# Kernel tuning notes

Hardware: AMD Instinct MI355X
Metric: run time of the kernel (lower is better)

Reference implementation:

```python
import jax, jax.numpy as jnp
import numpy as np
import math

HEAD_DIM = 32
N_Q_HEADS = 32
N_KV_HEADS = 8
ROPE_BASE = 10000.0
NEG_INF = -1e9


def _rope_cos_sin(seq_len, dtype):
    inv_freq = 1.0 / (ROPE_BASE ** (jnp.arange(0, HEAD_DIM, 2, dtype=jnp.float32) / HEAD_DIM))
    pos = jnp.arange(seq_len, dtype=jnp.float32)
    freqs = pos[:, None] * inv_freq[None, :]          # [S, D/2]
    emb = jnp.concatenate([freqs, freqs], axis=-1)     # [S, D]
    return jnp.cos(emb).astype(dtype), jnp.sin(emb).astype(dtype)


def _rotate_half(x):
    x1, x2 = jnp.split(x, 2, axis=-1)
    return jnp.concatenate([-x2, x1], axis=-1)


def _apply_rope(x, cos, sin):
    # x: [B, H, S, D]; cos/sin: [S, D]
    return x * cos[None, None] + _rotate_half(x) * sin[None, None]


def setup_inputs() -> dict:
    key = jax.random.key(0)
    ks = jax.random.split(key, 5)
    B, S, D = 2, 2048, 1024
    sc = 1.0 / math.sqrt(D)
    return {
        "hidden_states": jax.random.normal(ks[0], (B, S, D), jnp.float32),
        "attention_mask": jnp.ones((B, S), jnp.int32),
        "Wq": jax.random.normal(ks[1], (1024, 1024), jnp.float32) * sc,
        "Wk": jax.random.normal(ks[2], (256, 1024), jnp.float32) * sc,
        "Wv": jax.random.normal(ks[3], (256, 1024), jnp.float32) * sc,
        "Wo": jax.random.normal(ks[4], (1024, 1024), jnp.float32) * sc,
    }


def reference(hidden_states, attention_mask, Wq, Wk, Wv, Wo):
    B, S, D = hidden_states.shape
    group = N_Q_HEADS // N_KV_HEADS

    q = (hidden_states @ Wq.T).reshape(B, S, N_Q_HEADS, HEAD_DIM).transpose(0, 2, 1, 3)
    k = (hidden_states @ Wk.T).reshape(B, S, N_KV_HEADS, HEAD_DIM).transpose(0, 2, 1, 3)
    v = (hidden_states @ Wv.T).reshape(B, S, N_KV_HEADS, HEAD_DIM).transpose(0, 2, 1, 3)

    cos, sin = _rope_cos_sin(S, q.dtype)
    q = _apply_rope(q, cos, sin)
    k = _apply_rope(k, cos, sin)

    k = jnp.repeat(k, group, axis=1)  # [B, 32, S, D]
    v = jnp.repeat(v, group, axis=1)

    scores = jnp.einsum("bhqd,bhkd->bhqk", q, k) / math.sqrt(HEAD_DIM)

    causal = jnp.tril(jnp.ones((S, S), bool))
    allowed = causal[None, None] & (attention_mask[:, None, None, :] != 0)
    scores = jnp.where(allowed, scores, NEG_INF)

    attn = jax.nn.softmax(scores, axis=-1)
    out = jnp.einsum("bhqk,bhkd->bhqd", attn, v)  # [B, 32, S, 32]
    out = out.transpose(0, 2, 1, 3).reshape(B, S, D)
    return out @ Wo.T
```

## Files before the change

kernel.cpp:

```cpp
#include <hip/hip_runtime.h>

typedef __bf16 bf16x8 __attribute__((ext_vector_type(8)));
typedef __bf16 bf16x4 __attribute__((ext_vector_type(4)));
typedef short short4v __attribute__((ext_vector_type(4)));
typedef float f32x4 __attribute__((ext_vector_type(4)));

__device__ __forceinline__ f32x4 mfma16(bf16x8 a, bf16x8 b, f32x4 c) {
  return __builtin_amdgcn_mfma_f32_16x16x32_bf16(a, b, c, 0, 0, 0);
}

__device__ __forceinline__ f32x4 mfma16k16(bf16x4 a, bf16x4 b, f32x4 c) {
#if __has_builtin(__builtin_amdgcn_mfma_f32_16x16x16bf16_1k)
  short4v as = __builtin_bit_cast(short4v, a);
  short4v bs = __builtin_bit_cast(short4v, b);
  return __builtin_amdgcn_mfma_f32_16x16x16bf16_1k(as, bs, c, 0, 0, 0);
#else
  f32x4 d;
  asm volatile("v_mfma_f32_16x16x16_bf16 %0, %1, %2, %3"
               : "=v"(d)
               : "v"(a), "v"(b), "v"(c));
  return d;
#endif
}

__device__ __forceinline__ float fast_exp2(float x) {
  return __builtin_amdgcn_exp2f(x);
}

typedef const __attribute__((address_space(1))) void gvoid_t;
typedef __attribute__((address_space(3))) void svoid_t;
__device__ __forceinline__ void lds16(const __bf16* g, __bf16* l) {
  __builtin_amdgcn_global_load_lds((gvoid_t*)g, (svoid_t*)l, 16, 0, 0);
}

__global__ __launch_bounds__(256) void prep(const float* __restrict__ hidden,
                                            const float* __restrict__ Wq,
                                            const float* __restrict__ Wk,
                                            const float* __restrict__ Wv,
                                            const float* __restrict__ Wo,
                                            __bf16* __restrict__ hb,
                                            __bf16* __restrict__ Wqkvb,
                                            __bf16* __restrict__ Wob) {
  int q = blockIdx.x * 256 + threadIdx.x;
  const float* src;
  __bf16* dst;
  if (q < 1048576) {
    src = hidden; dst = hb;
  } else if ((q -= 1048576) < 262144) {
    src = Wq; dst = Wqkvb;
  } else if ((q -= 262144) < 65536) {
    src = Wk; dst = Wqkvb + 1048576;
  } else if ((q -= 65536) < 65536) {
    src = Wv; dst = Wqkvb + 1310720;
  } else {
    q -= 65536;
    src = Wo; dst = Wob;
  }
  float4 v = *(const float4*)(src + (size_t)q * 4);
  bf16x4 o = { (__bf16)v.x, (__bf16)v.y, (__bf16)v.z, (__bf16)v.w };
  *(bf16x4*)(dst + (size_t)q * 4) = o;
}

template <bool BF16_OUT>
__global__ __launch_bounds__(256) void gemm_nt(const __bf16* __restrict__ A,
                                               const __bf16* __restrict__ B,
                                               void* __restrict__ Cv, int N) {
  __shared__ __bf16 As[2][128][32];
  __shared__ __bf16 Bs[2][64][32];
  const int m0 = blockIdx.x * 128, n0 = blockIdx.y * 64;
  const int tid = threadIdx.x;
  const int wave = tid >> 6, lane = tid & 63, quad = lane >> 4, l16 = lane & 15;
  const int wr = wave >> 1, wc = wave & 1;
  const int srA = 32 * wave, srB = 16 * wave;
  const __bf16* Ag = A + (size_t)(m0 + srA + (lane >> 2)) * 1024 + (lane & 3) * 8;
  const __bf16* Bg = B + (size_t)(n0 + srB + (lane >> 2)) * 1024 + (lane & 3) * 8;
  f32x4 acc[4][2] = {};

  auto stage = [&](int buf, int k0) {
    lds16(Ag + k0, &As[buf][srA][0]);
    lds16(Ag + 16 * 1024 + k0, &As[buf][srA + 16][0]);
    lds16(Bg + k0, &Bs[buf][srB][0]);
  };
  stage(0, 0);
  __syncthreads();
  int buf = 0;
  for (int k0 = 0; k0 < 1024; k0 += 32) {
    if (k0 + 32 < 1024) stage(buf ^ 1, k0 + 32);
    bf16x8 af[4], bfr[2];
#pragma unroll
    for (int i = 0; i < 4; i++)
      af[i] = *(bf16x8*)&As[buf][64 * wr + 16 * i + l16][quad * 8];
#pragma unroll
    for (int j = 0; j < 2; j++)
      bfr[j] = *(bf16x8*)&Bs[buf][32 * wc + 16 * j + l16][quad * 8];
#pragma unroll
    for (int i = 0; i < 4; i++)
#pragma unroll
      for (int j = 0; j < 2; j++) acc[i][j] = mfma16(af[i], bfr[j], acc[i][j]);
    __syncthreads();
    buf ^= 1;
  }
#pragma unroll
  for (int i = 0; i < 4; i++)
#pragma unroll
    for (int j = 0; j < 2; j++)
#pragma unroll
      for (int r = 0; r < 4; r++) {
        int row = m0 + 64 * wr + 16 * i + quad * 4 + r;
        int col = n0 + 32 * wc + 16 * j + l16;
        if constexpr (BF16_OUT)
          ((__bf16*)Cv)[(size_t)row * N + col] = (__bf16)acc[i][j][r];
        else
          ((float*)Cv)[(size_t)row * N + col] = acc[i][j][r];
      }
}

__global__ __launch_bounds__(256) void ropevt(__bf16* __restrict__ QKV,
                                              __bf16* __restrict__ VT,
                                              const int* __restrict__ amask,
                                              float* __restrict__ maskb) {
  int idx = blockIdx.x * 256 + threadIdx.x;
  if (idx < 2621440) {
    __bf16* base;
    int m, i;
    if (idx < 2097152) {
      m = idx >> 9;
      int h = (idx >> 4) & 31;
      i = idx & 15;
      base = QKV + (size_t)m * 1536 + h * 32;
    } else {
      int j = idx - 2097152;
      m = j >> 7;
      int h = (j >> 4) & 7;
      i = j & 15;
      base = QKV + (size_t)m * 1536 + 1024 + h * 32;
    }
    int s = m & 2047;
    float inv = __expf(-(float)i * 0.5756462732485114f);
    float ang = (float)s * inv;
    float sn, cs;
    __sincosf(ang, &sn, &cs);
    float x0 = (float)base[i];
    float x1 = (float)base[i + 16];
    base[i] = (__bf16)(x0 * cs - x1 * sn);
    base[i + 16] = (__bf16)(x1 * cs + x0 * sn);
  } else {
    int j = idx - 2621440;
    if (j < 4096) maskb[j] = amask[j] ? -16.0f : -1.5e9f;
    int s4 = j & 511;
    int d = (j >> 9) & 31;
    int hb_ = j >> 14;
    int s = s4 * 4;
    int b_ = hb_ >> 3, hkv_ = hb_ & 7;
    const __bf16* src = QKV + (size_t)(b_ * 2048 + s) * 1536 + 1280 + hkv_ * 32 + d;
    bf16x4 ov = { src[0], src[1536], src[3072], src[4608] };
    *(bf16x4*)&VT[((size_t)hb_ * 32 + d) * 2048 + s] = ov;
  }
}

__global__ __launch_bounds__(256, 2) void attn(const __bf16* __restrict__ QKV,
                                               const __bf16* __restrict__ VT,
                                               const float* __restrict__ maskb,
                                               __bf16* __restrict__ Ob) {
  __shared__ __bf16 Ks[2][64][40];
  __shared__ __bf16 Vs[2][32][72];
  const int tid = threadIdx.x;
  const int wave = tid >> 6, lane = tid & 63;
  const int quad = lane >> 4, l16 = lane & 15;
  const int b = blockIdx.z, h = blockIdx.y, hkv = h >> 2;
  const int xp = blockIdx.x;
  const float SC2 = 0.25503472f;

  const int sk_key = tid >> 2, sk_ch = (tid & 3) * 8;
  const int sv_d = tid >> 3, sv_seg = (tid & 7) * 8;
  const __bf16* ksrc = QKV + (size_t)(b * 2048 + sk_key) * 1536 + 1024 + hkv * 32 + sk_ch;
  const __bf16* vsrc = VT + ((size_t)(b * 8 + hkv) * 32 + sv_d) * 2048 + sv_seg;
  const float* mrow = maskb + b * 2048;

  for (int sp = 0; sp < 2; sp++) {
    const int strip = sp ? 15 - xp : xp;
    const int qw = strip * 128 + wave * 32;
    const int q_row0 = qw + l16, q_row1 = qw + 16 + l16;
    const __bf16* qbase = QKV + (size_t)(b * 2048 + qw + l16) * 1536 + h * 32 + quad * 8;
    bf16x8 qf0 = *(const bf16x8*)qbase;
    bf16x8 qf1 = *(const bf16x8*)(qbase + 16 * 1536);

    {
      uint4 kr = *(const uint4*)ksrc;
      uint4 vr = *(const uint4*)vsrc;
      *(uint4*)&Ks[0][sk_key][sk_ch] = kr;
      *(uint4*)&Vs[0][sv_d][sv_seg] = vr;
    }
    __syncthreads();

    f32x4 o00 = {}, o01 = {}, o10 = {}, o11 = {};
    float rs0 = 0.f, rs1 = 0.f;
    int buf = 0;
    const int ntiles = 2 * strip + 2;

    for (int t = 0; t < ntiles; t++) {
      const int kv0 = t << 6;
      const bool more = (t + 1 < ntiles);
      uint4 kr, vr;
      if (more) {
        kr = *(const uint4*)(ksrc + (size_t)(t + 1) * 64 * 1536);
        vr = *(const uint4*)(vsrc + (size_t)(t + 1) * 64);
      }
      if (kv0 <= qw + 31) {
        bf16x8 kf[4];
#pragma unroll
        for (int kt = 0; kt < 4; kt++)
          kf[kt] = *(bf16x8*)&Ks[buf][16 * kt + l16][quad * 8];
        f32x4 s0[4], s1[4];
#pragma unroll
        for (int kt = 0; kt < 4; kt++) {
          f32x4 z = {};
          s0[kt] = mfma16(kf[kt], qf0, z);
          s1[kt] = mfma16(kf[kt], qf1, z);
        }
        bf16x4 pb0[4], pb1[4];
        if (kv0 + 63 <= qw) {
#pragma unroll
          for (int kt = 0; kt < 4; kt++) {
            const int kb = kv0 + 16 * kt + 4 * quad;
            float4 mb = *(const float4*)(mrow + kb);
#pragma unroll
            for (int r = 0; r < 4; r++) {
              float e0 = fast_exp2(fmaf(s0[kt][r], SC2, (&mb.x)[r]));
              float e1 = fast_exp2(fmaf(s1[kt][r], SC2, (&mb.x)[r]));
              rs0 += e0;
              rs1 += e1;
              pb0[kt][r] = (__bf16)e0;
              pb1[kt][r] = (__bf16)e1;
            }
          }
        } else {
#pragma unroll
          for (int kt = 0; kt < 4; kt++) {
            const int kb = kv0 + 16 * kt + 4 * quad;
            float4 mb = *(const float4*)(mrow + kb);
#pragma unroll
            for (int r = 0; r < 4; r++) {
              const int key = kb + r;
              float e0 = fast_exp2(fmaf(s0[kt][r], SC2, (&mb.x)[r]));
              float e1 = fast_exp2(fmaf(s1[kt][r], SC2, (&mb.x)[r]));
              e0 = (key <= q_row0) ? e0 : 0.f;
              e1 = (key <= q_row1) ? e1 : 0.f;
              rs0 += e0;
              rs1 += e1;
              pb0[kt][r] = (__bf16)e0;
              pb1[kt][r] = (__bf16)e1;
            }
          }
        }
#pragma unroll
        for (int kt = 0; kt < 4; kt++) {
          bf16x4 v0 = *(bf16x4*)&Vs[buf][l16][16 * kt + 4 * quad];
          bf16x4 v1 = *(bf16x4*)&Vs[buf][16 + l16][16 * kt + 4 * quad];
          o00 = mfma16k16(v0, pb0[kt], o00);
          o01 = mfma16k16(v1, pb0[kt], o01);
          o10 = mfma16k16(v0, pb1[kt], o10);
          o11 = mfma16k16(v1, pb1[kt], o11);
        }
      }
      if (more) {
        *(uint4*)&Ks[buf ^ 1][sk_key][sk_ch] = kr;
        *(uint4*)&Vs[buf ^ 1][sv_d][sv_seg] = vr;
      }
      __syncthreads();
      buf ^= 1;
    }
    rs0 += __shfl_xor(rs0, 16);
    rs0 += __shfl_xor(rs0, 32);
    rs1 += __shfl_xor(rs1, 16);
    rs1 += __shfl_xor(rs1, 32);
    float inv0 = 1.0f / rs0, inv1 = 1.0f / rs1;
    size_t row0 = (size_t)(b * 2048 + q_row0);
    size_t row1 = (size_t)(b * 2048 + q_row1);
    bf16x4 w00 = { (__bf16)(o00[0] * inv0), (__bf16)(o00[1] * inv0),
                   (__bf16)(o00[2] * inv0), (__bf16)(o00[3] * inv0) };
    bf16x4 w01 = { (__bf16)(o01[0] * inv0), (__bf16)(o01[1] * inv0),
                   (__bf16)(o01[2] * inv0), (__bf16)(o01[3] * inv0) };
    bf16x4 w10 = { (__bf16)(o10[0] * inv1), (__bf16)(o10[1] * inv1),
                   (__bf16)(o10[2] * inv1), (__bf16)(o10[3] * inv1) };
    bf16x4 w11 = { (__bf16)(o11[0] * inv1), (__bf16)(o11[1] * inv1),
                   (__bf16)(o11[2] * inv1), (__bf16)(o11[3] * inv1) };
    *(bf16x4*)&Ob[row0 * 1024 + h * 32 + quad * 4] = w00;
    *(bf16x4*)&Ob[row0 * 1024 + h * 32 + 16 + quad * 4] = w01;
    *(bf16x4*)&Ob[row1 * 1024 + h * 32 + quad * 4] = w10;
    *(bf16x4*)&Ob[row1 * 1024 + h * 32 + 16 + quad * 4] = w11;
  }
}

extern "C" void kernel_launch(void* const* d_in, const int* in_sizes, int n_in,
                              void* d_out, int out_size, void* d_ws, size_t ws_size,
                              hipStream_t stream) {
  const float* hidden = (const float*)d_in[0];
  const int* amask = (const int*)d_in[1];
  const float* Wq = (const float*)d_in[2];
  const float* Wk = (const float*)d_in[3];
  const float* Wv = (const float*)d_in[4];
  const float* Wo = (const float*)d_in[5];
  float* out = (float*)d_out;

  char* p = (char*)d_ws;
  auto carve = [&](size_t elems) {
    __bf16* r = (__bf16*)p;
    p += ((elems * 2 + 255) / 256) * 256;
    return r;
  };
  __bf16* hb = carve(4096ull * 1024);
  __bf16* Wqkvb = carve(1536ull * 1024);
  __bf16* Wob = carve(1024ull * 1024);
  __bf16* QKV = carve(4096ull * 1536);
  __bf16* VT = carve(4096ull * 256);
  __bf16* Ob = carve(4096ull * 1024);
  float* maskb = (float*)carve(8192);

  prep<<<6656, 256, 0, stream>>>(hidden, Wq, Wk, Wv, Wo, hb, Wqkvb, Wob);

  gemm_nt<true><<<dim3(32, 24), 256, 0, stream>>>(hb, Wqkvb, QKV, 1536);

  ropevt<<<11264, 256, 0, stream>>>(QKV, VT, amask, maskb);

  attn<<<dim3(8, 32, 2), 256, 0, stream>>>(QKV, VT, maskb, Ob);

  gemm_nt<false><<<dim3(32, 16), 256, 0, stream>>>(Ob, Wob, (void*)out, 1024);
}
```

Before: 199.7 us.

## Split attention KV range across two blocks, combine partials, enlarge GEMM tiles

Attention now divides each query strip's KV tiles into two halves handled by separate blocks. Each block writes unnormalized fp32 partial outputs and row sums, and a new combine kernel sums them, normalizes and writes bf16. This doubles the attention grid to improve occupancy and load balance, and occupancy is also raised to 4 blocks per SM. Separately, both GEMMs move to 128x128 tiles, giving more reuse per block but fewer blocks. The cost is an extra kernel and fp32 partial traffic of about 32 MB write plus read. It relies on the fixed max-free softmax, so the exp values can be summed across partials without rescaling.

```diff
diff --git a/kernel.cpp b/kernel.cpp
--- a/kernel.cpp
+++ b/kernel.cpp
@@ -66,48 +66,49 @@
                                                const __bf16* __restrict__ B,
                                                void* __restrict__ Cv, int N) {
   __shared__ __bf16 As[2][128][32];
-  __shared__ __bf16 Bs[2][64][32];
-  const int m0 = blockIdx.x * 128, n0 = blockIdx.y * 64;
+  __shared__ __bf16 Bs[2][128][32];
+  const int m0 = blockIdx.x * 128, n0 = blockIdx.y * 128;
   const int tid = threadIdx.x;
   const int wave = tid >> 6, lane = tid & 63, quad = lane >> 4, l16 = lane & 15;
   const int wr = wave >> 1, wc = wave & 1;
-  const int srA = 32 * wave, srB = 16 * wave;
-  const __bf16* Ag = A + (size_t)(m0 + srA + (lane >> 2)) * 1024 + (lane & 3) * 8;
-  const __bf16* Bg = B + (size_t)(n0 + srB + (lane >> 2)) * 1024 + (lane & 3) * 8;
-  f32x4 acc[4][2] = {};
+  const int srow = 32 * wave;
+  const __bf16* Ag = A + (size_t)(m0 + srow + (lane >> 2)) * 1024 + (lane & 3) * 8;
+  const __bf16* Bg = B + (size_t)(n0 + srow + (lane >> 2)) * 1024 + (lane & 3) * 8;
+  f32x4 acc[4][4] = {};
 
   auto stage = [&](int buf, int k0) {
-    lds16(Ag + k0, &As[buf][srA][0]);
-    lds16(Ag + 16 * 1024 + k0, &As[buf][srA + 16][0]);
-    lds16(Bg + k0, &Bs[buf][srB][0]);
+    lds16(Ag + k0, &As[buf][srow][0]);
+    lds16(Ag + 16 * 1024 + k0, &As[buf][srow + 16][0]);
+    lds16(Bg + k0, &Bs[buf][srow][0]);
+    lds16(Bg + 16 * 1024 + k0, &Bs[buf][srow + 16][0]);
   };
   stage(0, 0);
   __syncthreads();
   int buf = 0;
   for (int k0 = 0; k0 < 1024; k0 += 32) {
     if (k0 + 32 < 1024) stage(buf ^ 1, k0 + 32);
-    bf16x8 af[4], bfr[2];
+    bf16x8 af[4], bfr[4];
 #pragma unroll
     for (int i = 0; i < 4; i++)
       af[i] = *(bf16x8*)&As[buf][64 * wr + 16 * i + l16][quad * 8];
 #pragma unroll
-    for (int j = 0; j < 2; j++)
-      bfr[j] = *(bf16x8*)&Bs[buf][32 * wc + 16 * j + l16][quad * 8];
+    for (int j = 0; j < 4; j++)
+      bfr[j] = *(bf16x8*)&Bs[buf][64 * wc + 16 * j + l16][quad * 8];
 #pragma unroll
     for (int i = 0; i < 4; i++)
 #pragma unroll
-      for (int j = 0; j < 2; j++) acc[i][j] = mfma16(af[i], bfr[j], acc[i][j]);
+      for (int j = 0; j < 4; j++) acc[i][j] = mfma16(af[i], bfr[j], acc[i][j]);
     __syncthreads();
     buf ^= 1;
   }
 #pragma unroll
   for (int i = 0; i < 4; i++)
 #pragma unroll
-    for (int j = 0; j < 2; j++)
+    for (int j = 0; j < 4; j++)
 #pragma unroll
       for (int r = 0; r < 4; r++) {
         int row = m0 + 64 * wr + 16 * i + quad * 4 + r;
-        int col = n0 + 32 * wc + 16 * j + l16;
+        int col = n0 + 64 * wc + 16 * j + l16;
         if constexpr (BF16_OUT)
           ((__bf16*)Cv)[(size_t)row * N + col] = (__bf16)acc[i][j][r];
         else
@@ -158,17 +159,18 @@
   }
 }
 
-__global__ __launch_bounds__(256, 2) void attn(const __bf16* __restrict__ QKV,
+__global__ __launch_bounds__(256, 4) void attn(const __bf16* __restrict__ QKV,
                                                const __bf16* __restrict__ VT,
                                                const float* __restrict__ maskb,
-                                               __bf16* __restrict__ Ob) {
+                                               float* __restrict__ Opart,
+                                               float* __restrict__ rspart) {
   __shared__ __bf16 Ks[2][64][40];
   __shared__ __bf16 Vs[2][32][72];
   const int tid = threadIdx.x;
   const int wave = tid >> 6, lane = tid & 63;
   const int quad = lane >> 4, l16 = lane & 15;
   const int b = blockIdx.z, h = blockIdx.y, hkv = h >> 2;
-  const int xp = blockIdx.x;
+  const int xp = blockIdx.x >> 1, z = blockIdx.x & 1;
   const float SC2 = 0.25503472f;
 
   const int sk_key = tid >> 2, sk_ch = (tid & 3) * 8;
@@ -179,6 +181,8 @@
 
   for (int sp = 0; sp < 2; sp++) {
     const int strip = sp ? 15 - xp : xp;
+    const int t_begin = z ? (strip + 1) : 0;
+    const int t_end = z ? (2 * strip + 2) : (strip + 1);
     const int qw = strip * 128 + wave * 32;
     const int q_row0 = qw + l16, q_row1 = qw + 16 + l16;
     const __bf16* qbase = QKV + (size_t)(b * 2048 + qw + l16) * 1536 + h * 32 + quad * 8;
@@ -186,8 +190,8 @@
     bf16x8 qf1 = *(const bf16x8*)(qbase + 16 * 1536);
 
     {
-      uint4 kr = *(const uint4*)ksrc;
-      uint4 vr = *(const uint4*)vsrc;
+      uint4 kr = *(const uint4*)(ksrc + (size_t)t_begin * 64 * 1536);
+      uint4 vr = *(const uint4*)(vsrc + (size_t)t_begin * 64);
       *(uint4*)&Ks[0][sk_key][sk_ch] = kr;
       *(uint4*)&Vs[0][sv_d][sv_seg] = vr;
     }
@@ -196,11 +200,10 @@
     f32x4 o00 = {}, o01 = {}, o10 = {}, o11 = {};
     float rs0 = 0.f, rs1 = 0.f;
     int buf = 0;
-    const int ntiles = 2 * strip + 2;
-
-    for (int t = 0; t < ntiles; t++) {
+
+    for (int t = t_begin; t < t_end; t++) {
       const int kv0 = t << 6;
-      const bool more = (t + 1 < ntiles);
+      const bool more = (t + 1 < t_end);
       uint4 kr, vr;
       if (more) {
         kr = *(const uint4*)(ksrc + (size_t)(t + 1) * 64 * 1536);
@@ -214,9 +217,9 @@
         f32x4 s0[4], s1[4];
 #pragma unroll
         for (int kt = 0; kt < 4; kt++) {
-          f32x4 z = {};
-          s0[kt] = mfma16(kf[kt], qf0, z);
-          s1[kt] = mfma16(kf[kt], qf1, z);
+          f32x4 zz = {};
+          s0[kt] = mfma16(kf[kt], qf0, zz);
+          s1[kt] = mfma16(kf[kt], qf1, zz);
         }
         bf16x4 pb0[4], pb1[4];
         if (kv0 + 63 <= qw) {
@@ -274,22 +277,39 @@
     rs0 += __shfl_xor(rs0, 32);
     rs1 += __shfl_xor(rs1, 16);
     rs1 += __shfl_xor(rs1, 32);
-    float inv0 = 1.0f / rs0, inv1 = 1.0f / rs1;
+    float* Op = Opart + (size_t)z * 4096 * 1024;
     size_t row0 = (size_t)(b * 2048 + q_row0);
     size_t row1 = (size_t)(b * 2048 + q_row1);
-    bf16x4 w00 = { (__bf16)(o00[0] * inv0), (__bf16)(o00[1] * inv0),
-                   (__bf16)(o00[2] * inv0), (__bf16)(o00[3] * inv0) };
-    bf16x4 w01 = { (__bf16)(o01[0] * inv0), (__bf16)(o01[1] * inv0),
-                   (__bf16)(o01[2] * inv0), (__bf16)(o01[3] * inv0) };
-    bf16x4 w10 = { (__bf16)(o10[0] * inv1), (__bf16)(o10[1] * inv1),
-                   (__bf16)(o10[2] * inv1), (__bf16)(o10[3] * inv1) };
-    bf16x4 w11 = { (__bf16)(o11[0] * inv1), (__bf16)(o11[1] * inv1),
-                   (__bf16)(o11[2] * inv1), (__bf16)(o11[3] * inv1) };
-    *(bf16x4*)&Ob[row0 * 1024 + h * 32 + quad * 4] = w00;
-    *(bf16x4*)&Ob[row0 * 1024 + h * 32 + 16 + quad * 4] = w01;
-    *(bf16x4*)&Ob[row1 * 1024 + h * 32 + quad * 4] = w10;
-    *(bf16x4*)&Ob[row1 * 1024 + h * 32 + 16 + quad * 4] = w11;
+    *(f32x4*)&Op[row0 * 1024 + h * 32 + quad * 4] = o00;
+    *(f32x4*)&Op[row0 * 1024 + h * 32 + 16 + quad * 4] = o01;
+    *(f32x4*)&Op[row1 * 1024 + h * 32 + quad * 4] = o10;
+    *(f32x4*)&Op[row1 * 1024 + h * 32 + 16 + quad * 4] = o11;
+    if (quad == 0) {
+      size_t ri = ((size_t)(z * 2 + b) * 32 + h) * 2048;
+      rspart[ri + q_row0] = rs0;
+      rspart[ri + q_row1] = rs1;
+    }
   }
+}
+
+__global__ __launch_bounds__(256) void combine(const float* __restrict__ Opart,
+                                               const float* __restrict__ rspart,
+                                               __bf16* __restrict__ Ob) {
+  int idx = blockIdx.x * 256 + threadIdx.x;
+  int row = idx >> 7, g = idx & 127;
+  int b = row >> 11, q = row & 2047, h = g >> 2;
+  size_t off = (size_t)row * 1024 + g * 8;
+  float4 a0 = *(const float4*)(Opart + off);
+  float4 a1 = *(const float4*)(Opart + off + 4);
+  float4 c0 = *(const float4*)(Opart + 4194304 + off);
+  float4 c1 = *(const float4*)(Opart + 4194304 + off + 4);
+  size_t ri = ((size_t)b * 32 + h) * 2048 + q;
+  float inv = 1.0f / (rspart[ri] + rspart[2 * 65536 + ri]);
+  bf16x8 w = { (__bf16)((a0.x + c0.x) * inv), (__bf16)((a0.y + c0.y) * inv),
+               (__bf16)((a0.z + c0.z) * inv), (__bf16)((a0.w + c0.w) * inv),
+               (__bf16)((a1.x + c1.x) * inv), (__bf16)((a1.y + c1.y) * inv),
+               (__bf16)((a1.z + c1.z) * inv), (__bf16)((a1.w + c1.w) * inv) };
+  *(bf16x8*)&Ob[off] = w;
 }
 
 extern "C" void kernel_launch(void* const* d_in, const int* in_sizes, int n_in,
@@ -316,14 +336,18 @@
   __bf16* VT = carve(4096ull * 256);
   __bf16* Ob = carve(4096ull * 1024);
   float* maskb = (float*)carve(8192);
+  float* Opart = (float*)carve(2ull * 4096 * 1024 * 2);
+  float* rspart = (float*)carve(2ull * 2 * 32 * 2048 * 2);
 
   prep<<<6656, 256, 0, stream>>>(hidden, Wq, Wk, Wv, Wo, hb, Wqkvb, Wob);
 
-  gemm_nt<true><<<dim3(32, 24), 256, 0, stream>>>(hb, Wqkvb, QKV, 1536);
+  gemm_nt<true><<<dim3(32, 12), 256, 0, stream>>>(hb, Wqkvb, QKV, 1536);
 
   ropevt<<<11264, 256, 0, stream>>>(QKV, VT, amask, maskb);
 
-  attn<<<dim3(8, 32, 2), 256, 0, stream>>>(QKV, VT, maskb, Ob);
-
-  gemm_nt<false><<<dim3(32, 16), 256, 0, stream>>>(Ob, Wob, (void*)out, 1024);
-}
+  attn<<<dim3(16, 32, 2), 256, 0, stream>>>(QKV, VT, maskb, Opart, rspart);
+
+  combine<<<2048, 256, 0, stream>>>(Opart, rspart, Ob);
+
+  gemm_nt<false><<<dim3(32, 8), 256, 0, stream>>>(Ob, Wob, (void*)out, 1024);
+}
```

Measured after the change: 183.8 us. 1.09x faster.
